# Optimization experiments

Measured on AMD Instinct MI355X. Metric: run time of the kernel, lower is better.

Reference implementation:

```python
import jax, jax.numpy as jnp
import numpy as np

PI = np.pi
B_IN, B1, B2 = 30, 10, 6      # bandwidths: input S2, after conv1, after conv2
F1, F2, F_OUT = 20, 40, 10


def _wigner_d_stack(l, betas):
    """Wigner-d d^l_{mn}(beta) = <m|exp(-i beta Jy)|n> (real), shape [nbeta, 2l+1, 2l+1]."""
    n = 2 * l + 1
    m = np.arange(-l, l)
    c = np.sqrt(l * (l + 1) - m * (m + 1))          # J+ couplings m -> m+1
    Jp = np.zeros((n, n))
    Jp[np.arange(1, n), np.arange(n - 1)] = c
    A = 0.5 * (Jp.T - Jp)                            # exp(beta*A) = d^l(beta)
    ev, V = np.linalg.eig(A)
    Vi = np.linalg.inv(V)
    E = np.exp(np.multiply.outer(np.asarray(betas, np.float64), ev))
    return np.einsum('mk,bk,kn->bmn', V, E, Vi).real


def _qw(b):
    """Driscoll-Healy quadrature weights over beta for the SOFT grid of bandwidth b."""
    j = np.arange(2 * b)
    theta = PI * (2 * j + 1) / (4 * b)
    k = np.arange(b)
    return (2.0 / b) * np.sin(theta) * (np.sin(theta[:, None] * (2 * k + 1)) / (2 * k + 1)).sum(1)


def _betas(b):
    return PI * (2 * np.arange(2 * b) + 1) / (4 * b)


def _s2_grid():   # s2_near_identity_grid(): 3 betas x 8 alphas = 24 points
    beta = np.arange(1, 4) * (PI / 8) / 3
    alpha = np.linspace(0, 2 * PI, 8, endpoint=False)
    B, A = np.meshgrid(beta, alpha, indexing='ij')
    return B.ravel(), A.ravel()


def _so3_grid():  # so3_near_identity_grid(): 3x8x8 = 192 points, gamma = pre_gamma - alpha
    beta = np.arange(1, 4) * (PI / 8) / 3
    alpha = np.linspace(0, 2 * PI, 8, endpoint=False)
    pre_gamma = np.linspace(-2 * PI, 2 * PI, 8, endpoint=False)
    B, A, C = np.meshgrid(beta, alpha, pre_gamma, indexing='ij')
    return B.ravel(), A.ravel(), (C - A).ravel()


# ---------- static spectral constants (numpy, built once at import) ----------
_bet_in, _w_in = _betas(B_IN), _qw(B_IN)
_bet1, _w1 = _betas(B1), _qw(B1)
_bet2, _w2 = _betas(B2), _qw(B2)
_gb, _ga = _s2_grid()
_gb3, _ga3, _gc3 = _so3_grid()

# conv1 analysis: w(beta) * d^l_{m0}(beta_in), flattened over (l,m), l < B1
_dm1, _mi1, _y1 = [], [], []
for l in range(B1):
    d = _wigner_d_stack(l, _bet_in)                        # [60, 2l+1, 2l+1]
    _dm1.append((d[:, :, l] * _w_in[:, None]).T)           # [2l+1, 60] (column n=0)
    m = np.arange(-l, l + 1)
    _mi1.append(m % (2 * B_IN))
    dg = _wigner_d_stack(l, _gb)[:, :, l]                  # [24, 2l+1]
    _y1.append(np.exp(-1j * np.outer(m, _ga)) * dg.T)      # kernel rft basis [2l+1, 24]
DM1 = np.concatenate(_dm1, 0).astype(np.float32)           # [100, 60]
MI1 = np.concatenate(_mi1, 0)
Y1B = np.concatenate(_y1, 0).astype(np.complex64)          # [100, 24]

D_B1 = [_wigner_d_stack(l, _bet1) for l in range(B1)]      # d^l at the 20 betas of b=10 grid

# conv2 analysis: w(beta) * d^l_{mn}(beta_1), flattened over (l,m,n), l < B2
_dm2, _mi2, _ni2, _y2 = [], [], [], []
for l in range(B2):
    m = np.arange(-l, l + 1)
    d = D_B1[l]                                            # [20, 2l+1, 2l+1]
    _dm2.append((d * _w1[:, None, None]).reshape(2 * B1, -1).T)   # [(2l+1)^2, 20]
    mm, nn = np.meshgrid(m, m, indexing='ij')
    _mi2.append(mm.ravel() % (2 * B1))
    _ni2.append(nn.ravel() % (2 * B1))
    dg = _wigner_d_stack(l, _gb3)                          # [192, 2l+1, 2l+1]
    ph = np.exp(-1j * (np.multiply.outer(m, _ga3)[:, None, :] +
                       np.multiply.outer(m, _gc3)[None, :, :]))   # [2l+1,2l+1,192]
    _y2.append((np.moveaxis(dg, 0, -1) * ph).reshape(-1, _gb3.size))
DM2 = np.concatenate(_dm2, 0).astype(np.float32)           # [286, 20]
MI2 = np.concatenate(_mi2, 0)
NI2 = np.concatenate(_ni2, 0)
Y2B = np.concatenate(_y2, 0).astype(np.complex64)          # [286, 192]

D_B1F = [d.astype(np.float32) for d in D_B1]
D_B2F = [_wigner_d_stack(l, _bet2).astype(np.float32) for l in range(B2)]

SC1 = np.float32(1.0 / np.sqrt(_gb.size * 1))    # kernel scalings (s2cnn-style init scale)
SC2 = np.float32(1.0 / np.sqrt(_gb3.size * F1))
W2J = _w2.astype(np.float32)
INTEG_SCALE = np.float32((2 * PI / (2 * B2)) ** 2)


def _forward(x, kernel1, kernel2, w_out, bias_out):
    Bt = x.shape[0]
    # ---- S2Convolution: S2-FFT(x), rft(kernel), s2_mm, SO3-iFFT ----
    xh = jnp.fft.fft(x, axis=-1) / (2 * B_IN)                     # [B,1,60,60] cplx (alpha FFT)
    xg = xh[..., jnp.asarray(MI1)]                                # [B,1,60,100]
    X = jnp.einsum('kj,bfjk->kbf', jnp.asarray(DM1), xg)          # [100,B,1] spectral F^l_m
    Yk = jnp.einsum('kg,iog->kio', jnp.asarray(Y1B), kernel1.astype(jnp.complex64)) * SC1
    S = jnp.zeros((Bt, F1, 2 * B1, 2 * B1, 2 * B1), jnp.complex64)
    off = 0
    for l in range(B1):
        L = 2 * l + 1
        Z = jnp.einsum('mbi,nio->mnbo', X[off:off + L], jnp.conj(Yk[off:off + L]))
        T = jnp.einsum('jmn,mnbo->bojmn', float(2 * l + 1) * jnp.asarray(D_B1F[l]), Z)
        mi = np.arange(-l, l + 1) % (2 * B1)
        S = S.at[:, :, :, mi[:, None], mi[None, :]].add(T)
        off += L
    x1 = jnp.fft.ifft2(S, axes=(-2, -1)).real * float((2 * B1) ** 2)   # [B,F1,20,20,20]
    x1 = jax.nn.relu(x1)
    # ---- SO3Convolution: SO3-FFT, rft(kernel), so3_mm, SO3-iFFT ----
    xh2 = jnp.fft.fft2(x1, axes=(-2, -1)) / float((2 * B1) ** 2)       # alpha,gamma FFT
    xg2 = xh2[:, :, :, jnp.asarray(MI2), jnp.asarray(NI2)]             # [B,F1,20,286]
    X2 = jnp.einsum('kj,bfjk->kbf', jnp.asarray(DM2), xg2)             # [286,B,F1]
    Yk2 = jnp.einsum('kg,iog->kio', jnp.asarray(Y2B), kernel2.astype(jnp.complex64)) * SC2
    S2 = jnp.zeros((Bt, F2, 2 * B2, 2 * B2, 2 * B2), jnp.complex64)
    off = 0
    for l in range(B2):
        L = 2 * l + 1
        X2l = X2[off:off + L * L].reshape(L, L, Bt, F1)     # [m,k,B,i]
        Y2l = Yk2[off:off + L * L].reshape(L, L, F1, F2)    # [n,k,i,o]
        Z = jnp.einsum('mkbi,nkio->mnbo', X2l, jnp.conj(Y2l))   # hat z^l = hat x^l hat y^l+
        T = jnp.einsum('jmn,mnbo->bojmn', float(2 * l + 1) * jnp.asarray(D_B2F[l]), Z)
        mi = np.arange(-l, l + 1) % (2 * B2)
        S2 = S2.at[:, :, :, mi[:, None], mi[None, :]].add(T)
        off += L * L
    x2 = jnp.fft.ifft2(S2, axes=(-2, -1)).real * float((2 * B2) ** 2)  # [B,F2,12,12,12]
    x2 = jax.nn.relu(x2)
    # ---- so3_integrate + linear head ----
    feat = INTEG_SCALE * jnp.einsum('bfjac,j->bf', x2, jnp.asarray(W2J))
    return feat @ w_out.T + bias_out


def setup_inputs() -> dict:
    key = jax.random.key(0)
    ks = jax.random.split(key, 5)
    return {
        'x': jax.random.normal(ks[0], (128, 1, 2 * B_IN, 2 * B_IN), jnp.float32),
        'kernel1': jax.random.normal(ks[1], (1, F1, 24), jnp.float32),
        'kernel2': jax.random.normal(ks[2], (F1, F2, 192), jnp.float32),
        'w_out': jax.random.normal(ks[3], (F_OUT, F2), jnp.float32) / np.sqrt(float(F2)),
        'bias_out': jax.random.normal(ks[4], (F_OUT,), jnp.float32) * 0.01,
    }


def reference(x, kernel1, kernel2, w_out, bias_out):
    return _forward(x, kernel1, kernel2, w_out, bias_out)
```

## Files before the change

### kernel.cpp

```cpp
#include <hip/hip_runtime.h>
#include <cmath>

#define NT 256
#define BT 128

#define OFF_W60   0
#define OFF_E20   2280
#define OFF_E12   2320
#define OFF_W2J   2344
#define OFF_DM1   2356
#define OFF_Y1B   8356
#define OFF_D1R   13156
#define OFF_DM2   39756
#define OFF_Y2B   45476
#define OFF_D2R   155300
#define OFF_T19U  158732
#define OFF_T11V  159492
#define OFF_T12U  159932
#define OFF_TABA  160196
#define OFF_TABB  161526
#define OFF_TH19  161812
#define OFF_TH12  162212
#define OFF_TABH  162356
#define OFF_TAH1  162504
#define OFF_DM2T  163220
#define OFF_TGIX  168940
#define OFF_END   169228
#define N_INIT    109735

__constant__ int c_ZB1[10] = {0,1,10,35,84,165,286,455,680,969};
__constant__ int c_ZBH[10] = {0,1,7,22,50,95,161,252,372,525};
__constant__ int c_ZB2[6]  = {0,1,10,35,84,165};
__constant__ int c_BOFF[6] = {0,22,208,718,1712,3350};

__device__ inline void wsync() {
    __asm__ volatile("" ::: "memory");
    __builtin_amdgcn_s_waitcnt(0xC07F);
    __builtin_amdgcn_wave_barrier();
    __asm__ volatile("" ::: "memory");
}

__device__ inline double dipow(double x, int e) {
    double r = 1.0;
    for (int i = 0; i < e; ++i) r *= x;
    return r;
}

__device__ double wigd(const double* F, const double* Fi, int l, int mp, int m, double beta) {
    double cb = cos(beta * 0.5), sb = sin(beta * 0.5);
    int smin = m - mp; if (smin < 0) smin = 0;
    int smax = l + m;  if (l - mp < smax) smax = l - mp;
    double pref = sqrt(F[l+mp] * F[l-mp] * F[l+m] * F[l-m]);
    double sum = 0.0;
    for (int s = smin; s <= smax; ++s) {
        double t = pref * (Fi[l+m-s] * Fi[s] * Fi[mp-m+s] * Fi[l-mp-s]);
        t *= dipow(cb, 2*l + m - mp - 2*s) * dipow(sb, mp - m + 2*s);
        sum += ((mp - m + s) & 1) ? -t : t;
    }
    return sum;
}

__device__ double qwj(int bnd, int j) {
    const double PI = 3.14159265358979323846;
    double theta = PI * (2*j + 1) / (4.0 * bnd);
    double s = 0.0;
    for (int k = 0; k < bnd; ++k) s += sin(theta * (2*k + 1)) / (2*k + 1);
    return 2.0 / bnd * sin(theta) * s;
}

__global__ void k_init(float* __restrict__ ws) {
    int idx = blockIdx.x * blockDim.x + threadIdx.x;
    if (idx >= N_INIT) return;
    double F[20], Fi[20];
    F[0] = 1.0;
    #pragma unroll
    for (int i = 1; i < 20; ++i) F[i] = F[i-1] * i;
    Fi[19] = 1.0 / F[19];
    #pragma unroll
    for (int i = 18; i >= 0; --i) Fi[i] = Fi[i+1] * (i+1);
    const double PI = 3.14159265358979323846;

    if (idx < 1140) {
        int r = idx / 60, a = idx % 60;
        double ang = -2.0 * PI * (double)((r - 9) * a) / 60.0;
        ws[OFF_W60 + 2*idx]     = (float)cos(ang);
        ws[OFF_W60 + 2*idx + 1] = (float)sin(ang);
    } else if (idx < 1160) {
        int t = idx - 1140;
        double ang = 2.0 * PI * t / 20.0;
        ws[OFF_E20 + 2*t]     = (float)cos(ang);
        ws[OFF_E20 + 2*t + 1] = (float)sin(ang);
    } else if (idx < 1172) {
        int t = idx - 1160;
        double ang = 2.0 * PI * t / 12.0;
        ws[OFF_E12 + 2*t]     = (float)cos(ang);
        ws[OFF_E12 + 2*t + 1] = (float)sin(ang);
    } else if (idx < 1184) {
        int j = idx - 1172;
        ws[OFF_W2J + j] = (float)qwj(6, j);
    } else if (idx < 7184) {
        int e = idx - 1184; int k = e / 60, j = e % 60;
        int l = 0; while ((l + 1) * (l + 1) <= k) ++l;
        int m = k - l*l - l;
        double beta = PI * (2*j + 1) / 120.0;
        ws[OFF_DM1 + e] = (float)(qwj(30, j) * wigd(F, Fi, l, m, 0, beta));
    } else if (idx < 9584) {
        int e = idx - 7184; int k = e / 24, g = e % 24;
        int l = 0; while ((l + 1) * (l + 1) <= k) ++l;
        int m = k - l*l - l;
        int bi = g / 8, ai = g % 8;
        double beta  = (bi + 1) * (PI / 8.0) / 3.0;
        double alpha = 2.0 * PI * ai / 8.0;
        double d = wigd(F, Fi, l, m, 0, beta);
        double ph = -(double)m * alpha;
        ws[OFF_Y1B + 2*e]     = (float)(d * cos(ph));
        ws[OFF_Y1B + 2*e + 1] = (float)(d * sin(ph));
    } else if (idx < 36184) {
        int e = idx - 9584; int j = e / 1330, t = e % 1330;
        int l = 0; while (l < 9 && t >= c_ZB1[l+1]) ++l;
        int L = 2*l + 1, loc = t - c_ZB1[l];
        int mi = loc / L, ni = loc % L;
        double beta = PI * (2*j + 1) / 40.0;
        ws[OFF_D1R + e] = (float)((double)L * wigd(F, Fi, l, mi - l, ni - l, beta));
    } else if (idx < 41904) {
        int e = idx - 36184; int j = e / 286, k2 = e % 286;
        int l = 0; while (l < 5 && k2 >= c_ZB2[l+1]) ++l;
        int L = 2*l + 1, loc = k2 - c_ZB2[l];
        int mi = loc / L, ni = loc % L;
        double beta = PI * (2*j + 1) / 40.0;
        ws[OFF_DM2 + e] = (float)(qwj(10, j) * wigd(F, Fi, l, mi - l, ni - l, beta));
    } else if (idx < 96816) {
        int e = idx - 41904; int k2 = e / 192, g = e % 192;
        int l = 0; while (l < 5 && k2 >= c_ZB2[l+1]) ++l;
        int L = 2*l + 1, loc = k2 - c_ZB2[l];
        int m = loc / L - l, n = loc % L - l;
        int bi = g / 64, ai = (g / 8) % 8, ci = g % 8;
        double beta  = (bi + 1) * (PI / 8.0) / 3.0;
        double alpha = 2.0 * PI * ai / 8.0;
        double gamma = (-2.0 * PI + ci * (PI / 2.0)) - alpha;
        double d = wigd(F, Fi, l, m, n, beta);
        double ph = -((double)m * alpha + (double)n * gamma);
        ws[OFF_Y2B + 2*e]     = (float)(d * cos(ph));
        ws[OFF_Y2B + 2*e + 1] = (float)(d * sin(ph));
    } else if (idx < 100248) {
        int e = idx - 96816; int j = e / 286, t = e % 286;
        int l = 0; while (l < 5 && t >= c_ZB2[l+1]) ++l;
        int L = 2*l + 1, loc = t - c_ZB2[l];
        int mi = loc / L, ni = loc % L;
        double beta = PI * (2*j + 1) / 24.0;
        ws[OFF_D2R + e] = (float)((double)L * wigd(F, Fi, l, mi - l, ni - l, beta));
    } else if (idx < 100628) {
        int e = idx - 100248; int c = e / 19, n = e % 19 - 9;
        double ang = 2.0 * PI * (double)(n * c) / 20.0;
        ws[OFF_T19U + 2*e]     = (float)cos(ang);
        ws[OFF_T19U + 2*e + 1] = (float)sin(ang);
    } else if (idx < 100848) {
        int e = idx - 100628; int r = e / 20, c = e % 20;
        double ang = -2.0 * PI * (double)((r - 5) * c) / 20.0;
        ws[OFF_T11V + 2*e]     = (float)cos(ang);
        ws[OFF_T11V + 2*e + 1] = (float)sin(ang);
    } else if (idx < 100980) {
        int e = idx - 100848; int c = e / 11, n = e % 11 - 5;
        double ang = 2.0 * PI * (double)(n * c) / 12.0;
        ws[OFF_T12U + 2*e]     = (float)cos(ang);
        ws[OFF_T12U + 2*e + 1] = (float)sin(ang);
    } else if (idx < 102310) {
        int t = idx - 100980;
        int l = 0; while (l < 9 && t >= c_ZB1[l+1]) ++l;
        int L = 2*l + 1, loc = t - c_ZB1[l];
        ((int*)ws)[OFF_TABA + t] = l | ((loc / L) << 8) | ((loc % L) << 16);
    } else if (idx < 102596) {
        int t = idx - 102310;
        int l = 0; while (l < 5 && t >= c_ZB2[l+1]) ++l;
        int L = 2*l + 1, loc = t - c_ZB2[l];
        ((int*)ws)[OFF_TABB + t] = l | ((loc / L) << 8) | ((loc % L) << 16);
    } else if (idx < 102796) {
        int e = idx - 102596; int a = e / 10, mm = e % 10;
        double f = (mm == 0) ? 1.0 : 2.0;
        double ang = 2.0 * PI * (double)(mm * a) / 20.0;
        ws[OFF_TH19 + 2*e]     = (float)(f * cos(ang));
        ws[OFF_TH19 + 2*e + 1] = (float)(f * sin(ang));
    } else if (idx < 102868) {
        int e = idx - 102796; int a = e / 6, mm = e % 6;
        double f = (mm == 0) ? 1.0 : 2.0;
        double ang = 2.0 * PI * (double)(mm * a) / 12.0;
        ws[OFF_TH12 + 2*e]     = (float)(f * cos(ang));
        ws[OFF_TH12 + 2*e + 1] = (float)(f * sin(ang));
    } else if (idx < 103014) {
        int t = idx - 102868;
        int l = 0, cum = 0, loc = 0;
        for (; l < 6; ++l) {
            int L = 2*l + 1, h = (L*L + 1) / 2;
            if (t < cum + h) { loc = t - cum; break; }
            cum += h;
        }
        ((int*)ws)[OFF_TABH + t] = l | (loc << 8);
    } else if (idx < 103729) {
        int t = idx - 103014;
        int l = 0; while (l < 9 && t >= c_ZBH[l+1]) ++l;
        int L = 2*l + 1, loc = t - c_ZBH[l];
        ((int*)ws)[OFF_TAH1 + t] = l | ((loc / L) << 8) | ((loc % L) << 16);
    } else if (idx < 109449) {
        int e = idx - 103729; int k2 = e / 20, j = e % 20;
        int l = 0; while (l < 5 && k2 >= c_ZB2[l+1]) ++l;
        int L = 2*l + 1, loc = k2 - c_ZB2[l];
        int mi = loc / L, ni = loc % L;
        double beta = PI * (2*j + 1) / 40.0;
        ws[OFF_DM2T + e] = (float)(qwj(10, j) * wigd(F, Fi, l, mi - l, ni - l, beta) / 400.0);
    } else {
        int t = idx - 109449;
        int l = 0; while (l < 5 && t >= c_ZB2[l+1]) ++l;
        int L = 2*l + 1, loc = t - c_ZB2[l];
        int m = loc / L - l, n = loc % L - l;
        int gi, sgbit;
        if (m >= 0) { gi = m * 11 + (n + 5); sgbit = 0; }
        else        { gi = (-m) * 11 + (5 - n); sgbit = 1; }
        ((int*)ws)[OFF_TGIX + t] = gi | (sgbit << 16);
    }
}

__global__ void k_dft_alpha(const float* __restrict__ x, const float2* __restrict__ W60,
                            float2* __restrict__ xh) {
    int idx = blockIdx.x * blockDim.x + threadIdx.x;
    if (idx >= BT * 60 * 19) return;
    int r = idx % 19;
    int j = (idx / 19) % 60;
    int b = idx / (19 * 60);
    const float* xr = x + (b * 60 + j) * 60;
    const float2* wr = W60 + r * 60;
    float re = 0.f, im = 0.f;
    for (int a = 0; a < 60; ++a) {
        float v = xr[a];
        float2 w = wr[a];
        re += v * w.x; im += v * w.y;
    }
    xh[idx] = make_float2(re * (1.f / 60.f), im * (1.f / 60.f));
}

__global__ void k_X1(const float2* __restrict__ xh, const float* __restrict__ DM1,
                     float2* __restrict__ X) {
    int idx = blockIdx.x * blockDim.x + threadIdx.x;
    if (idx >= 100 * BT) return;
    int b = idx % BT, k = idx / BT;
    int l = 0; while ((l + 1) * (l + 1) <= k) ++l;
    int r = (k - l*l - l) + 9;
    float re = 0.f, im = 0.f;
    for (int j = 0; j < 60; ++j) {
        float d = DM1[k * 60 + j];
        float2 v = xh[(b * 60 + j) * 19 + r];
        re += d * v.x; im += d * v.y;
    }
    X[k * BT + b] = make_float2(re, im);
}

__global__ void k_Yk1(const float* __restrict__ k1, const float2* __restrict__ Y1B,
                      float2* __restrict__ Yk1) {
    int idx = blockIdx.x * blockDim.x + threadIdx.x;
    if (idx >= 100 * 20) return;
    int o = idx % 20, k = idx / 20;
    float re = 0.f, im = 0.f;
    for (int g = 0; g < 24; ++g) {
        float2 y = Y1B[k * 24 + g];
        float w = k1[o * 24 + g];
        re += y.x * w; im += y.y * w;
    }
    const float SC1 = 0.20412414523193154f;
    Yk1[idx] = make_float2(re * SC1, im * SC1);
}

__global__ __launch_bounds__(NT) void k_Yk2(const float* __restrict__ k2in,
                                            const float2* __restrict__ Y2B,
                                            const int* __restrict__ gTABH,
                                            float2* __restrict__ Yk2) {
    const int h = blockIdx.x >> 1;
    const int half = blockIdx.x & 1;
    const int tid = threadIdx.x;
    int ph = gTABH[h];
    int l = ph & 255, loc = ph >> 8;
    int L = 2 * l + 1;
    int mi = loc / L, ni = loc % L;
    int k2  = c_ZB2[l] + loc;
    int locm = L * L - 1 - loc;
    int k2m = c_ZB2[l] + locm;
    float par = ((mi + ni) & 1) ? -1.f : 1.f;

    __shared__ __align__(16) float2 sY[192];
    for (int t = tid; t < 192; t += NT) sY[t] = Y2B[k2 * 192 + t];
    __syncthreads();
    const float4* sY4 = (const float4*)sY;
    const float SC2 = 0.016137430609197573f;
    for (int t = half * 400 + tid; t < half * 400 + 400; t += NT) {
        int o = t / 20, i = t % 20;
        const float4* kp = (const float4*)(k2in + (i * 40 + o) * 192);
        float re = 0.f, im = 0.f;
        #pragma unroll 4
        for (int p = 0; p < 48; ++p) {
            float4 w = kp[p];
            float4 y01 = sY4[2*p], y23 = sY4[2*p + 1];
            re += w.x * y01.x + w.y * y01.z + w.z * y23.x + w.w * y23.z;
            im += w.x * y01.y + w.y * y01.w + w.z * y23.y + w.w * y23.w;
        }
        re *= SC2; im *= SC2;
        Yk2[(o * 286 + k2) * 20 + i] = make_float2(re, im);
        if (k2m != k2)
            Yk2[(o * 286 + k2m) * 20 + i] = make_float2(par * re, -par * im);
    }
}

__global__ __launch_bounds__(NT) void k_stage1(
    const float2* __restrict__ X, const float2* __restrict__ Yk1,
    const float* __restrict__ gD1R,
    const float2* __restrict__ gT19, const float2* __restrict__ gT11,
    const float2* __restrict__ gTH19,
    const int* __restrict__ gTAH1, float2* __restrict__ Gg) {
    const int b = blockIdx.x % BT;
    const int f = blockIdx.x / BT;
    const int tid = threadIdx.x;
    const int wv = tid >> 6, lane = tid & 63;

    __shared__ __align__(16) float2 sZ[715];
    __shared__ __align__(16) float2 sT19[440];
    __shared__ __align__(16) float2 sTH19[280];
    __shared__ __align__(16) float2 sT11[220];
    __shared__ __align__(16) float2 sA[4][224];
    __shared__ __align__(16) float2 sB[4][280];

    for (int t = tid; t < 380; t += NT) sT19[(t / 19) * 22 + (t % 19)] = gT19[t];
    for (int t = tid; t < 200; t += NT) sTH19[(t / 10) * 14 + (t % 10)] = gTH19[t];
    for (int t = tid; t < 220; t += NT) sT11[t] = gT11[t];
    for (int t = tid; t < 715; t += NT) {
        int p = gTAH1[t];
        int l = p & 255, mm = (p >> 8) & 255, ni = p >> 16;
        float2 a = X[(l*l + l + mm) * BT + b];
        float2 y = Yk1[(l*l + ni) * 20 + f];
        sZ[t] = make_float2(a.x * y.x + a.y * y.y, a.y * y.x - a.x * y.y);
    }
    __syncthreads();

    float2* S   = sA[wv];
    float2* U   = sB[wv];
    float*  x1  = (float*)sA[wv];
    float2* V   = sB[wv];

    for (int jj = 0; jj < 5; ++jj) {
        const int j = wv + 4 * jj;

        {
            const float* dp = gD1R + j * 1330;
            for (int t = lane; t < 190; t += 64) {
                int mm = t / 19, ni = t % 19;
                int n = ni - 9;
                int an = n < 0 ? -n : n;
                int lmin = mm > an ? mm : an;
                float re = 0.f, im = 0.f;
                for (int l = lmin; l < 10; ++l) {
                    int L = 2*l + 1;
                    float dv = dp[c_ZB1[l] + (mm + l) * L + (n + l)];
                    float2 z = sZ[c_ZBH[l] + mm * L + (n + l)];
                    re += dv * z.x; im += dv * z.y;
                }
                S[mm * 22 + ni] = make_float2(re, im);
            }
        }
        wsync();

        for (int t = lane; t < 200; t += 64) {
            int mm = t / 20, c = t % 20;
            const float4* sp = (const float4*)(S + mm * 22);
            const float4* tp = (const float4*)(sT19 + c * 22);
            float re = 0.f, im = 0.f;
            #pragma unroll
            for (int p = 0; p < 9; ++p) {
                float4 s = sp[p], w = tp[p];
                re += s.x * w.x - s.y * w.y + s.z * w.z - s.w * w.w;
                im += s.x * w.y + s.y * w.x + s.z * w.w + s.w * w.z;
            }
            float2 s1 = S[mm * 22 + 18], w1 = sT19[c * 22 + 18];
            re += s1.x * w1.x - s1.y * w1.y;
            im += s1.x * w1.y + s1.y * w1.x;
            U[c * 14 + mm] = make_float2(re, im);
        }
        wsync();

        for (int t = lane; t < 200; t += 64) {
            int cp = t % 10, a = t / 10;
            const float4* u0 = (const float4*)(U + cp * 14);
            const float4* u1 = (const float4*)(U + (cp + 10) * 14);
            const float4* tp = (const float4*)(sTH19 + a * 14);
            float s0a = 0.f, s0b = 0.f, s1a = 0.f, s1b = 0.f;
            #pragma unroll
            for (int p = 0; p < 5; ++p) {
                float4 w = tp[p];
                float4 ua = u0[p], ub = u1[p];
                s0a += ua.x * w.x - ua.y * w.y;
                s0b += ua.z * w.z - ua.w * w.w;
                s1a += ub.x * w.x - ub.y * w.y;
                s1b += ub.z * w.z - ub.w * w.w;
            }
            float v0 = s0a + s0b, v1 = s1a + s1b;
            x1[a * 20 + cp]      = v0 > 0.f ? v0 : 0.f;
            x1[a * 20 + cp + 10] = v1 > 0.f ? v1 : 0.f;
        }
        wsync();

        for (int t = lane; t < 120; t += 64) {
            int nn = t / 20, a = t % 20;
            const float4* xp = (const float4*)(x1 + a * 20);
            const float4* tp = (const float4*)(sT11 + (nn + 5) * 20);
            float r0 = 0.f, i0 = 0.f, r1 = 0.f, i1 = 0.f;
            #pragma unroll
            for (int p = 0; p < 5; ++p) {
                float4 xv = xp[p];
                float4 t01 = tp[2*p], t23 = tp[2*p + 1];
                r0 += xv.x * t01.x + xv.y * t01.z;
                i0 += xv.x * t01.y + xv.y * t01.w;
                r1 += xv.z * t23.x + xv.w * t23.z;
                i1 += xv.z * t23.y + xv.w * t23.w;
            }
            V[nn * 22 + a] = make_float2(r0 + r1, i0 + i1);
        }
        wsync();

        for (int t = lane; t < 66; t += 64) {
            int mm = t / 11, ni2 = t % 11;
            int nn2 = ni2 - 5;
            int na = nn2 < 0 ? -nn2 : nn2;
            float s = nn2 < 0 ? -1.f : 1.f;
            const float4* vp = (const float4*)(V + na * 22);
            const float4* tp = (const float4*)(sT11 + (mm + 5) * 20);
            float r0 = 0.f, i0 = 0.f, r1 = 0.f, i1 = 0.f;
            #pragma unroll
            for (int q = 0; q < 10; ++q) {
                float4 v = vp[q], w = tp[q];
                float vy0 = s * v.y, vy1 = s * v.w;
                r0 += v.x * w.x - vy0 * w.y;
                i0 += v.x * w.y + vy0 * w.x;
                r1 += v.z * w.z - vy1 * w.w;
                i1 += v.z * w.w + vy1 * w.z;
            }
            Gg[((size_t)(b * 20 + f) * 20 + j) * 66 + t] = make_float2(r0 + r1, i0 + i1);
        }
        wsync();
    }
}

__global__ __launch_bounds__(NT) void k_X2c(
    const float2* __restrict__ Gg, const float* __restrict__ gDM2T,
    const int* __restrict__ gTGIX, float2* __restrict__ X2g) {
    const int b = blockIdx.x % BT;
    const int f = blockIdx.x / BT;
    const int tid = threadIdx.x;
    __shared__ __align__(16) float2 sG[1320];
    const float2* Gp = Gg + (size_t)(b * 20 + f) * 20 * 66;
    for (int t = tid; t < 1320; t += NT) sG[t] = Gp[t];
    __syncthreads();
    for (int k2 = tid; k2 < 286; k2 += NT) {
        int e = gTGIX[k2];
        int gi = e & 0xFFFF;
        float sg = (e >> 16) ? -1.f : 1.f;
        const float* dm = gDM2T + k2 * 20;
        float re = 0.f, im = 0.f;
        #pragma unroll
        for (int j = 0; j < 20; ++j) {
            float d = dm[j];
            float2 g = sG[j * 66 + gi];
            re += d * g.x; im += d * g.y;
        }
        X2g[b * 5720 + k2 * 20 + f] = make_float2(re, sg * im);
    }
}

__global__ __launch_bounds__(NT) void k_Z2(
    const float2* __restrict__ X2g, const float2* __restrict__ Yk2,
    const int* __restrict__ gTABB, const int* __restrict__ gTABH,
    float2* __restrict__ Z2g) {
    const int bt = blockIdx.x & 15;
    const int o  = blockIdx.x >> 4;
    const int b0 = bt * 8;
    const int tid = threadIdx.x;

    __shared__ __align__(16) float2 sB[5792];

    const float2* Bg = Yk2 + o * 5720;
    for (int e = tid; e < 5720; e += NT) {
        int k2 = e / 20, i = e % 20;
        int p = gTABB[k2];
        int l = p & 255, r = (p >> 8) & 255, kk = p >> 16;
        sB[c_BOFF[l] + r * (40 * l + 22) + kk * 20 + i] = Bg[e];
    }
    __syncthreads();

    for (int q = tid; q < 8 * 146; q += NT) {
        int b_local = q / 146, h = q % 146;
        int ph = gTABH[h];
        int l = ph & 255, loc = ph >> 8;
        int L = 2 * l + 1;
        int mi = loc / L, ni = loc % L;
        const float4* ap = (const float4*)(X2g + (size_t)(b0 + b_local) * 5720
                                           + (c_ZB2[l] + mi * L) * 20);
        const float4* bp = (const float4*)(sB + c_BOFF[l] + ni * (40 * l + 22));
        float re = 0.f, im = 0.f;
        int n4 = 10 * L;
        for (int p4 = 0; p4 < n4; ++p4) {
            float4 a = ap[p4], y = bp[p4];
            re += a.x * y.x + a.y * y.y + a.z * y.z + a.w * y.w;
            im += a.y * y.x - a.x * y.y + a.w * y.z - a.z * y.w;
        }
        size_t base = ((size_t)(b0 + b_local) * 40 + o) * 286;
        Z2g[base + c_ZB2[l] + loc] = make_float2(re, im);
        int locm = L * L - 1 - loc;
        if (locm != loc) {
            float sg = ((mi + ni) & 1) ? -1.f : 1.f;
            Z2g[base + c_ZB2[l] + locm] = make_float2(sg * re, -sg * im);
        }
    }
}

__global__ __launch_bounds__(NT) void k_stage2b(
    const float2* __restrict__ Z2g, const float* __restrict__ gD2R,
    const float2* __restrict__ gT12, const float2* __restrict__ gTH12,
    const float* __restrict__ gW2J, float* __restrict__ feat) {
    const int b = blockIdx.x % BT;
    const int o = blockIdx.x / BT;
    const int tid = threadIdx.x;
    const int wv = tid >> 6, lane = tid & 63;

    __shared__ __align__(16) float2 sZb[286];
    __shared__ __align__(16) float2 sT12[168];
    __shared__ __align__(16) float2 sTH12[96];
    __shared__ __align__(16) float2 sS[4][88];
    __shared__ __align__(16) float2 sU[4][96];
    __shared__ float sredw[4];

    const float2* Zr = Z2g + ((size_t)b * 40 + o) * 286;
    for (int t = tid; t < 286; t += NT) sZb[t] = Zr[t];
    for (int t = tid; t < 132; t += NT) sT12[(t / 11) * 14 + (t % 11)] = gT12[t];
    for (int t = tid; t < 72; t += NT) sTH12[(t / 6) * 8 + (t % 6)] = gTH12[t];
    __syncthreads();

    float2* S = sS[wv];
    float2* U = sU[wv];
    float facc = 0.f;

    for (int jj = 0; jj < 3; ++jj) {
        const int j = wv + 4 * jj;

        {
            const float* dp = gD2R + j * 286;
            for (int t = lane; t < 66; t += 64) {
                int mm = t / 11, ni = t % 11;
                int n = ni - 5;
                int an = n < 0 ? -n : n;
                int lmin = mm > an ? mm : an;
                float re = 0.f, im = 0.f;
                for (int l = lmin; l < 6; ++l) {
                    int L = 2*l + 1;
                    int off = c_ZB2[l] + (mm + l) * L + (n + l);
                    float dv = dp[off];
                    float2 z = sZb[off];
                    re += dv * z.x; im += dv * z.y;
                }
                S[mm * 14 + ni] = make_float2(re, im);
            }
        }
        wsync();

        for (int t = lane; t < 72; t += 64) {
            int mm = t / 12, c = t % 12;
            const float4* sp = (const float4*)(S + mm * 14);
            const float4* tp = (const float4*)(sT12 + c * 14);
            float re = 0.f, im = 0.f;
            #pragma unroll
            for (int p = 0; p < 5; ++p) {
                float4 s = sp[p], w = tp[p];
                re += s.x * w.x - s.y * w.y + s.z * w.z - s.w * w.w;
                im += s.x * w.y + s.y * w.x + s.z * w.w + s.w * w.z;
            }
            float2 s1 = S[mm * 14 + 10], w1 = sT12[c * 14 + 10];
            re += s1.x * w1.x - s1.y * w1.y;
            im += s1.x * w1.y + s1.y * w1.x;
            U[c * 8 + mm] = make_float2(re, im);
        }
        wsync();

        {
            float wj = gW2J[j];
            for (int t = lane; t < 144; t += 64) {
                int a = t / 12, c = t % 12;
                const float4* up = (const float4*)(U + c * 8);
                const float4* tp = (const float4*)(sTH12 + a * 8);
                float acc = 0.f;
                #pragma unroll
                for (int p = 0; p < 3; ++p) {
                    float4 u = up[p], w = tp[p];
                    acc += u.x * w.x - u.y * w.y + u.z * w.z - u.w * w.w;
                }
                if (acc > 0.f) facc += wj * acc;
            }
        }
        wsync();
    }

    #pragma unroll
    for (int d = 32; d > 0; d >>= 1) facc += __shfl_down(facc, d, 64);
    if (lane == 0) sredw[wv] = facc;
    __syncthreads();
    if (tid == 0) {
        const float INTEG = 0.27415567780803774f;
        feat[b * 40 + o] = (sredw[0] + sredw[1] + sredw[2] + sredw[3]) * INTEG;
    }
}

__global__ void k_out(const float* __restrict__ feat, const float* __restrict__ w,
                      const float* __restrict__ bias, float* __restrict__ out) {
    int idx = blockIdx.x * blockDim.x + threadIdx.x;
    if (idx >= BT * 10) return;
    int fo = idx % 10, b = idx / 10;
    float acc = bias[fo];
    for (int o2 = 0; o2 < 40; ++o2) acc += feat[b * 40 + o2] * w[fo * 40 + o2];
    out[idx] = acc;
}

extern "C" void kernel_launch(void* const* d_in, const int* in_sizes, int n_in,
                              void* d_out, int out_size, void* d_ws, size_t ws_size,
                              hipStream_t stream) {
    (void)in_sizes; (void)n_in; (void)out_size; (void)ws_size;
    const float* x   = (const float*)d_in[0];
    const float* k1  = (const float*)d_in[1];
    const float* k2  = (const float*)d_in[2];
    const float* wO  = (const float*)d_in[3];
    const float* bO  = (const float*)d_in[4];
    float* out = (float*)d_out;

    float* ws = (float*)d_ws;
    const float2* cW60 = (const float2*)(ws + OFF_W60);
    const float*  cW2J = ws + OFF_W2J;
    const float*  cDM1 = ws + OFF_DM1;
    const float2* cY1B = (const float2*)(ws + OFF_Y1B);
    const float*  gD1R = ws + OFF_D1R;
    const float2* cY2B = (const float2*)(ws + OFF_Y2B);
    const float*  gD2R = ws + OFF_D2R;
    const float2* gT19 = (const float2*)(ws + OFF_T19U);
    const float2* gT11 = (const float2*)(ws + OFF_T11V);
    const float2* gT12 = (const float2*)(ws + OFF_T12U);
    const float2* gTH19 = (const float2*)(ws + OFF_TH19);
    const float2* gTH12 = (const float2*)(ws + OFF_TH12);
    const int*    gTABB = (const int*)(ws + OFF_TABB);
    const int*    gTABH = (const int*)(ws + OFF_TABH);
    const int*    gTAH1 = (const int*)(ws + OFF_TAH1);
    const float*  gDM2T = ws + OFF_DM2T;
    const int*    gTGIX = (const int*)(ws + OFF_TGIX);

    float2* xh   = (float2*)(ws + OFF_END);
    float2* X    = xh + BT * 60 * 19;
    float2* Yk1  = X + 100 * BT;
    float2* Yk2  = Yk1 + 100 * 20;
    float2* X2   = Yk2 + 40 * 286 * 20;
    float*  feat = (float*)(X2 + (size_t)BT * 5720);
    float2* Gg   = (float2*)(feat + BT * 40);
    float2* Z2   = Gg;

    k_init<<<(N_INIT + NT - 1) / NT, NT, 0, stream>>>(ws);
    k_dft_alpha<<<(BT * 60 * 19 + NT - 1) / NT, NT, 0, stream>>>(x, cW60, xh);
    k_X1<<<(100 * BT + NT - 1) / NT, NT, 0, stream>>>(xh, cDM1, X);
    k_Yk1<<<(100 * 20 + NT - 1) / NT, NT, 0, stream>>>(k1, cY1B, Yk1);
    k_Yk2<<<292, NT, 0, stream>>>(k2, cY2B, gTABH, Yk2);
    k_stage1<<<BT * 20, NT, 0, stream>>>(X, Yk1, gD1R, gT19, gT11, gTH19, gTAH1, Gg);
    k_X2c<<<BT * 20, NT, 0, stream>>>(Gg, gDM2T, gTGIX, X2);
    k_Z2<<<640, NT, 0, stream>>>(X2, Yk2, gTABB, gTABH, Z2);
    k_stage2b<<<BT * 40, NT, 0, stream>>>(Z2, gD2R, gT12, gTH12, cW2J, feat);
    k_out<<<(BT * 10 + NT - 1) / NT, NT, 0, stream>>>(feat, wO, bO, out);
}
```

Baseline: 437.9 us.

## Factor init tables, fuse X1/Yk1, split Z2 work, use real-DFT symmetry in stage1

The one-time table init is split into two kernels. The first precomputes quadrature weights, small-beta Wigner-d values and phase tables, so the large Y2B table is built by multiplication instead of per-entry wigd and trig calls. Unused tables (DM2, TABA) are no longer filled. The X1 and Yk1 kernels are merged into one launch, and k_Z2 is split into two halves by l so each block stages less shared memory and twice as many blocks run. In stage1 the size-20 inverse DFTs use an even/odd split, so each thread produces two outputs and half the loop iterations are needed.

```diff
diff --git a/kernel.cpp b/kernel.cpp
--- a/kernel.cpp
+++ b/kernel.cpp
@@ -25,8 +25,15 @@
 #define OFF_TAH1  162504
 #define OFF_DM2T  163220
 #define OFF_TGIX  168940
-#define OFF_END   169228
-#define N_INIT    109735
+#define OFF_QW30  169228
+#define OFF_QW10  169288
+#define OFF_QW6   169308
+#define OFF_D3B   169320
+#define OFF_PA    170178
+#define OFF_PG    170354
+#define OFF_END   171764
+#define N_INIT1   1742
+#define N_INIT2   109735
 
 __constant__ int c_ZB1[10] = {0,1,10,35,84,165,286,455,680,969};
 __constant__ int c_ZBH[10] = {0,1,7,22,50,95,161,252,372,525};
@@ -68,9 +75,49 @@
     return 2.0 / bnd * sin(theta) * s;
 }
 
-__global__ void k_init(float* __restrict__ ws) {
+__global__ void k_init1(float* __restrict__ ws) {
     int idx = blockIdx.x * blockDim.x + threadIdx.x;
-    if (idx >= N_INIT) return;
+    if (idx >= N_INIT1) return;
+    double F[20], Fi[20];
+    F[0] = 1.0;
+    #pragma unroll
+    for (int i = 1; i < 20; ++i) F[i] = F[i-1] * i;
+    Fi[19] = 1.0 / F[19];
+    #pragma unroll
+    for (int i = 18; i >= 0; --i) Fi[i] = Fi[i+1] * (i+1);
+    const double PI = 3.14159265358979323846;
+
+    if (idx < 60) {
+        ws[OFF_QW30 + idx] = (float)qwj(30, idx);
+    } else if (idx < 80) {
+        ws[OFF_QW10 + idx - 60] = (float)qwj(10, idx - 60);
+    } else if (idx < 92) {
+        ws[OFF_QW6 + idx - 80] = (float)qwj(6, idx - 80);
+    } else if (idx < 950) {
+        int e = idx - 92; int k2 = e / 3, bi = e % 3;
+        int l = 0; while (l < 5 && k2 >= c_ZB2[l+1]) ++l;
+        int L = 2*l + 1, loc = k2 - c_ZB2[l];
+        int m = loc / L - l, n = loc % L - l;
+        double beta = (bi + 1) * (PI / 8.0) / 3.0;
+        ws[OFF_D3B + e] = (float)wigd(F, Fi, l, m, n, beta);
+    } else if (idx < 1038) {
+        int e = idx - 950; int m = e / 8 - 5, ai = e % 8;
+        double ph = -(double)m * (2.0 * PI * ai / 8.0);
+        ws[OFF_PA + 2*e]     = (float)cos(ph);
+        ws[OFF_PA + 2*e + 1] = (float)sin(ph);
+    } else {
+        int e = idx - 1038; int n = e / 64 - 5, g2 = e % 64, ai = g2 / 8, ci = g2 % 8;
+        double alpha = 2.0 * PI * ai / 8.0;
+        double gamma = (-2.0 * PI + ci * (PI / 2.0)) - alpha;
+        double ph = -(double)n * gamma;
+        ws[OFF_PG + 2*e]     = (float)cos(ph);
+        ws[OFF_PG + 2*e + 1] = (float)sin(ph);
+    }
+}
+
+__global__ void k_init2(float* __restrict__ ws) {
+    int idx = blockIdx.x * blockDim.x + threadIdx.x;
+    if (idx >= N_INIT2) return;
     double F[20], Fi[20];
     F[0] = 1.0;
     #pragma unroll
@@ -97,13 +144,13 @@
         ws[OFF_E12 + 2*t + 1] = (float)sin(ang);
     } else if (idx < 1184) {
         int j = idx - 1172;
-        ws[OFF_W2J + j] = (float)qwj(6, j);
+        ws[OFF_W2J + j] = ws[OFF_QW6 + j];
     } else if (idx < 7184) {
         int e = idx - 1184; int k = e / 60, j = e % 60;
         int l = 0; while ((l + 1) * (l + 1) <= k) ++l;
         int m = k - l*l - l;
         double beta = PI * (2*j + 1) / 120.0;
-        ws[OFF_DM1 + e] = (float)(qwj(30, j) * wigd(F, Fi, l, m, 0, beta));
+        ws[OFF_DM1 + e] = (float)((double)ws[OFF_QW30 + j] * wigd(F, Fi, l, m, 0, beta));
     } else if (idx < 9584) {
         int e = idx - 7184; int k = e / 24, g = e % 24;
         int l = 0; while ((l + 1) * (l + 1) <= k) ++l;
@@ -123,25 +170,17 @@
         double beta = PI * (2*j + 1) / 40.0;
         ws[OFF_D1R + e] = (float)((double)L * wigd(F, Fi, l, mi - l, ni - l, beta));
     } else if (idx < 41904) {
-        int e = idx - 36184; int j = e / 286, k2 = e % 286;
-        int l = 0; while (l < 5 && k2 >= c_ZB2[l+1]) ++l;
-        int L = 2*l + 1, loc = k2 - c_ZB2[l];
-        int mi = loc / L, ni = loc % L;
-        double beta = PI * (2*j + 1) / 40.0;
-        ws[OFF_DM2 + e] = (float)(qwj(10, j) * wigd(F, Fi, l, mi - l, ni - l, beta));
     } else if (idx < 96816) {
         int e = idx - 41904; int k2 = e / 192, g = e % 192;
         int l = 0; while (l < 5 && k2 >= c_ZB2[l+1]) ++l;
         int L = 2*l + 1, loc = k2 - c_ZB2[l];
         int m = loc / L - l, n = loc % L - l;
         int bi = g / 64, ai = (g / 8) % 8, ci = g % 8;
-        double beta  = (bi + 1) * (PI / 8.0) / 3.0;
-        double alpha = 2.0 * PI * ai / 8.0;
-        double gamma = (-2.0 * PI + ci * (PI / 2.0)) - alpha;
-        double d = wigd(F, Fi, l, m, n, beta);
-        double ph = -((double)m * alpha + (double)n * gamma);
-        ws[OFF_Y2B + 2*e]     = (float)(d * cos(ph));
-        ws[OFF_Y2B + 2*e + 1] = (float)(d * sin(ph));
+        float d = ws[OFF_D3B + k2 * 3 + bi];
+        const float2 pa = ((const float2*)(ws + OFF_PA))[(m + 5) * 8 + ai];
+        const float2 pg = ((const float2*)(ws + OFF_PG))[(n + 5) * 64 + ai * 8 + ci];
+        ws[OFF_Y2B + 2*e]     = d * (pa.x * pg.x - pa.y * pg.y);
+        ws[OFF_Y2B + 2*e + 1] = d * (pa.x * pg.y + pa.y * pg.x);
     } else if (idx < 100248) {
         int e = idx - 96816; int j = e / 286, t = e % 286;
         int l = 0; while (l < 5 && t >= c_ZB2[l+1]) ++l;
@@ -165,10 +204,6 @@
         ws[OFF_T12U + 2*e]     = (float)cos(ang);
         ws[OFF_T12U + 2*e + 1] = (float)sin(ang);
     } else if (idx < 102310) {
-        int t = idx - 100980;
-        int l = 0; while (l < 9 && t >= c_ZB1[l+1]) ++l;
-        int L = 2*l + 1, loc = t - c_ZB1[l];
-        ((int*)ws)[OFF_TABA + t] = l | ((loc / L) << 8) | ((loc % L) << 16);
     } else if (idx < 102596) {
         int t = idx - 102310;
         int l = 0; while (l < 5 && t >= c_ZB2[l+1]) ++l;
@@ -206,7 +241,8 @@
         int L = 2*l + 1, loc = k2 - c_ZB2[l];
         int mi = loc / L, ni = loc % L;
         double beta = PI * (2*j + 1) / 40.0;
-        ws[OFF_DM2T + e] = (float)(qwj(10, j) * wigd(F, Fi, l, mi - l, ni - l, beta) / 400.0);
+        ws[OFF_DM2T + e] = (float)((double)ws[OFF_QW10 + j] *
+                                   wigd(F, Fi, l, mi - l, ni - l, beta) / 400.0);
     } else {
         int t = idx - 109449;
         int l = 0; while (l < 5 && t >= c_ZB2[l+1]) ++l;
@@ -237,35 +273,36 @@
     xh[idx] = make_float2(re * (1.f / 60.f), im * (1.f / 60.f));
 }
 
-__global__ void k_X1(const float2* __restrict__ xh, const float* __restrict__ DM1,
-                     float2* __restrict__ X) {
-    int idx = blockIdx.x * blockDim.x + threadIdx.x;
-    if (idx >= 100 * BT) return;
-    int b = idx % BT, k = idx / BT;
-    int l = 0; while ((l + 1) * (l + 1) <= k) ++l;
-    int r = (k - l*l - l) + 9;
-    float re = 0.f, im = 0.f;
-    for (int j = 0; j < 60; ++j) {
-        float d = DM1[k * 60 + j];
-        float2 v = xh[(b * 60 + j) * 19 + r];
-        re += d * v.x; im += d * v.y;
-    }
-    X[k * BT + b] = make_float2(re, im);
-}
-
-__global__ void k_Yk1(const float* __restrict__ k1, const float2* __restrict__ Y1B,
-                      float2* __restrict__ Yk1) {
-    int idx = blockIdx.x * blockDim.x + threadIdx.x;
-    if (idx >= 100 * 20) return;
-    int o = idx % 20, k = idx / 20;
-    float re = 0.f, im = 0.f;
-    for (int g = 0; g < 24; ++g) {
-        float2 y = Y1B[k * 24 + g];
-        float w = k1[o * 24 + g];
-        re += y.x * w; im += y.y * w;
-    }
-    const float SC1 = 0.20412414523193154f;
-    Yk1[idx] = make_float2(re * SC1, im * SC1);
+__global__ void k_X1Y1(const float2* __restrict__ xh, const float* __restrict__ DM1,
+                       float2* __restrict__ X, const float* __restrict__ k1,
+                       const float2* __restrict__ Y1B, float2* __restrict__ Yk1) {
+    int bid = blockIdx.x;
+    if (bid < 50) {
+        int idx = bid * NT + threadIdx.x;
+        if (idx >= 100 * BT) return;
+        int b = idx % BT, k = idx / BT;
+        int l = 0; while ((l + 1) * (l + 1) <= k) ++l;
+        int r = (k - l*l - l) + 9;
+        float re = 0.f, im = 0.f;
+        for (int j = 0; j < 60; ++j) {
+            float d = DM1[k * 60 + j];
+            float2 v = xh[(b * 60 + j) * 19 + r];
+            re += d * v.x; im += d * v.y;
+        }
+        X[k * BT + b] = make_float2(re, im);
+    } else {
+        int idx = (bid - 50) * NT + threadIdx.x;
+        if (idx >= 100 * 20) return;
+        int o = idx % 20, k = idx / 20;
+        float re = 0.f, im = 0.f;
+        for (int g = 0; g < 24; ++g) {
+            float2 y = Y1B[k * 24 + g];
+            float w = k1[o * 24 + g];
+            re += y.x * w; im += y.y * w;
+        }
+        const float SC1 = 0.20412414523193154f;
+        Yk1[idx] = make_float2(re * SC1, im * SC1);
+    }
 }
 
 __global__ __launch_bounds__(NT) void k_Yk2(const float* __restrict__ k2in,
@@ -364,42 +401,47 @@
         }
         wsync();
 
-        for (int t = lane; t < 200; t += 64) {
-            int mm = t / 20, c = t % 20;
+        for (int t = lane; t < 100; t += 64) {
+            int mm = t / 10, c = t % 10;
             const float4* sp = (const float4*)(S + mm * 22);
             const float4* tp = (const float4*)(sT19 + c * 22);
-            float re = 0.f, im = 0.f;
+            float re_e = 0.f, im_e = 0.f, re_o = 0.f, im_o = 0.f;
             #pragma unroll
             for (int p = 0; p < 9; ++p) {
                 float4 s = sp[p], w = tp[p];
-                re += s.x * w.x - s.y * w.y + s.z * w.z - s.w * w.w;
-                im += s.x * w.y + s.y * w.x + s.z * w.w + s.w * w.z;
-            }
-            float2 s1 = S[mm * 22 + 18], w1 = sT19[c * 22 + 18];
-            re += s1.x * w1.x - s1.y * w1.y;
-            im += s1.x * w1.y + s1.y * w1.x;
-            U[c * 14 + mm] = make_float2(re, im);
+                re_o += s.x * w.x - s.y * w.y;  im_o += s.x * w.y + s.y * w.x;
+                re_e += s.z * w.z - s.w * w.w;  im_e += s.z * w.w + s.w * w.z;
+            }
+            {
+                float2 s1 = S[mm * 22 + 18], w1 = sT19[c * 22 + 18];
+                re_o += s1.x * w1.x - s1.y * w1.y;
+                im_o += s1.x * w1.y + s1.y * w1.x;
+            }
+            U[c * 14 + mm]        = make_float2(re_e + re_o, im_e + im_o);
+            U[(c + 10) * 14 + mm] = make_float2(re_e - re_o, im_e - im_o);
         }
         wsync();
 
-        for (int t = lane; t < 200; t += 64) {
-            int cp = t % 10, a = t / 10;
+        for (int t = lane; t < 100; t += 64) {
+            int cp = t % 10, ap = t / 10;
             const float4* u0 = (const float4*)(U + cp * 14);
             const float4* u1 = (const float4*)(U + (cp + 10) * 14);
-            const float4* tp = (const float4*)(sTH19 + a * 14);
-            float s0a = 0.f, s0b = 0.f, s1a = 0.f, s1b = 0.f;
+            const float4* tp = (const float4*)(sTH19 + ap * 14);
+            float e0 = 0.f, o0 = 0.f, e1 = 0.f, o1 = 0.f;
             #pragma unroll
             for (int p = 0; p < 5; ++p) {
                 float4 w = tp[p];
                 float4 ua = u0[p], ub = u1[p];
-                s0a += ua.x * w.x - ua.y * w.y;
-                s0b += ua.z * w.z - ua.w * w.w;
-                s1a += ub.x * w.x - ub.y * w.y;
-                s1b += ub.z * w.z - ub.w * w.w;
-            }
-            float v0 = s0a + s0b, v1 = s1a + s1b;
-            x1[a * 20 + cp]      = v0 > 0.f ? v0 : 0.f;
-            x1[a * 20 + cp + 10] = v1 > 0.f ? v1 : 0.f;
+                e0 += ua.x * w.x - ua.y * w.y;
+                o0 += ua.z * w.z - ua.w * w.w;
+                e1 += ub.x * w.x - ub.y * w.y;
+                o1 += ub.z * w.z - ub.w * w.w;
+            }
+            float v;
+            v = e0 + o0; x1[ap * 20 + cp]             = v > 0.f ? v : 0.f;
+            v = e0 - o0; x1[(ap + 10) * 20 + cp]      = v > 0.f ? v : 0.f;
+            v = e1 + o1; x1[ap * 20 + cp + 10]        = v > 0.f ? v : 0.f;
+            v = e1 - o1; x1[(ap + 10) * 20 + cp + 10] = v > 0.f ? v : 0.f;
         }
         wsync();
 
@@ -474,31 +516,37 @@
     const float2* __restrict__ X2g, const float2* __restrict__ Yk2,
     const int* __restrict__ gTABB, const int* __restrict__ gTABH,
     float2* __restrict__ Z2g) {
-    const int bt = blockIdx.x & 15;
-    const int o  = blockIdx.x >> 4;
+    const int bt   = blockIdx.x & 15;
+    const int part = (blockIdx.x >> 4) & 1;
+    const int o    = blockIdx.x >> 5;
     const int b0 = bt * 8;
     const int tid = threadIdx.x;
 
-    __shared__ __align__(16) float2 sB[5792];
-
-    const float2* Bg = Yk2 + o * 5720;
-    for (int e = tid; e < 5720; e += NT) {
-        int k2 = e / 20, i = e % 20;
+    __shared__ __align__(16) float2 sB[3350];
+
+    const int sub  = part ? 3350 : 0;
+    const int stN  = part ? 2420 : 3300;
+    const int k2b  = part ? 165 : 0;
+    const float2* Bg = Yk2 + o * 5720 + k2b * 20;
+    for (int e = tid; e < stN; e += NT) {
+        int k2 = k2b + e / 20, i = e % 20;
         int p = gTABB[k2];
         int l = p & 255, r = (p >> 8) & 255, kk = p >> 16;
-        sB[c_BOFF[l] + r * (40 * l + 22) + kk * 20 + i] = Bg[e];
+        sB[c_BOFF[l] - sub + r * (40 * l + 22) + kk * 20 + i] = Bg[e];
     }
     __syncthreads();
 
-    for (int q = tid; q < 8 * 146; q += NT) {
-        int b_local = q / 146, h = q % 146;
+    const int perb  = part ? 61 : 85;
+    const int hbase = part ? 85 : 0;
+    for (int q = tid; q < 8 * perb; q += NT) {
+        int b_local = q / perb, h = hbase + q % perb;
         int ph = gTABH[h];
         int l = ph & 255, loc = ph >> 8;
         int L = 2 * l + 1;
         int mi = loc / L, ni = loc % L;
         const float4* ap = (const float4*)(X2g + (size_t)(b0 + b_local) * 5720
                                            + (c_ZB2[l] + mi * L) * 20);
-        const float4* bp = (const float4*)(sB + c_BOFF[l] + ni * (40 * l + 22));
+        const float4* bp = (const float4*)(sB + c_BOFF[l] - sub + ni * (40 * l + 22));
         float re = 0.f, im = 0.f;
         int n4 = 10 * L;
         for (int p4 = 0; p4 < n4; ++p4) {
@@ -660,14 +708,14 @@
     float2* Gg   = (float2*)(feat + BT * 40);
     float2* Z2   = Gg;
 
-    k_init<<<(N_INIT + NT - 1) / NT, NT, 0, stream>>>(ws);
+    k_init1<<<(N_INIT1 + NT - 1) / NT, NT, 0, stream>>>(ws);
+    k_init2<<<(N_INIT2 + NT - 1) / NT, NT, 0, stream>>>(ws);
     k_dft_alpha<<<(BT * 60 * 19 + NT - 1) / NT, NT, 0, stream>>>(x, cW60, xh);
-    k_X1<<<(100 * BT + NT - 1) / NT, NT, 0, stream>>>(xh, cDM1, X);
-    k_Yk1<<<(100 * 20 + NT - 1) / NT, NT, 0, stream>>>(k1, cY1B, Yk1);
+    k_X1Y1<<<58, NT, 0, stream>>>(xh, cDM1, X, k1, cY1B, Yk1);
     k_Yk2<<<292, NT, 0, stream>>>(k2, cY2B, gTABH, Yk2);
     k_stage1<<<BT * 20, NT, 0, stream>>>(X, Yk1, gD1R, gT19, gT11, gTH19, gTAH1, Gg);
     k_X2c<<<BT * 20, NT, 0, stream>>>(Gg, gDM2T, gTGIX, X2);
-    k_Z2<<<640, NT, 0, stream>>>(X2, Yk2, gTABB, gTABH, Z2);
+    k_Z2<<<1280, NT, 0, stream>>>(X2, Yk2, gTABB, gTABH, Z2);
     k_stage2b<<<BT * 40, NT, 0, stream>>>(Z2, gD2R, gT12, gTH12, cW2J, feat);
     k_out<<<(BT * 10 + NT - 1) / NT, NT, 0, stream>>>(feat, wO, bO, out);
 }
```

Result: faster. 397.5 us (-9.2%).
